# Kernel optimization log

Hardware: AMD Instinct MI355X
Metric: run time of the kernel (lower is better)

Reference implementation:

```python
import jax, jax.numpy as jnp
import numpy as np

# Static DAG: input -> L hidden layers of K nodes (dense between layers) -> output.
B, WIDTH, K, L = 262144, 64, 4, 4


def _linear_init(key, shape, fan_in):
    # matches nn.Linear default: U(-1/sqrt(fan_in), 1/sqrt(fan_in))
    bound = 1.0 / np.sqrt(fan_in)
    return jax.random.uniform(key, shape, jnp.float32, -bound, bound)


def setup_inputs() -> dict:
    key = jax.random.key(0)
    ks = jax.random.split(key, 9)
    x = jax.random.normal(ks[0], (B, WIDTH), jnp.float32)
    # input node -> first hidden layer (K edges)
    W_in = _linear_init(ks[1], (K, WIDTH, WIDTH), WIDTH)
    b_in = _linear_init(ks[2], (K, WIDTH), WIDTH)
    # between hidden layers: (L-1) transitions, K*K edges each; [pred, node, out, in]
    W_mid = _linear_init(ks[3], (L - 1, K, K, WIDTH, WIDTH), WIDTH)
    b_mid = _linear_init(ks[4], (L - 1, K, K, WIDTH), WIDTH)
    # last hidden layer -> output node (K edges)
    W_out = _linear_init(ks[5], (K, WIDTH, WIDTH), WIDTH)
    b_out = _linear_init(ks[6], (K, WIDTH), WIDTH)
    return {"x": x, "W_in": W_in, "b_in": b_in, "W_mid": W_mid,
            "b_mid": b_mid, "W_out": W_out, "b_out": b_out}


def _l2_normalize(t):
    # torch.linalg.norm(t) with no dim: Frobenius norm over the WHOLE tensor
    return t / jnp.linalg.norm(t)


def reference(x, W_in, b_in, W_mid, b_mid, W_out, b_out):
    # input node -> layer 1: each node k gets a single edge Linear, then normalize
    h = jnp.einsum('bw,kvw->kbv', x, W_in) + b_in[:, None, :]  # [K,B,W]
    h = jax.vmap(_l2_normalize)(h)
    # hidden -> hidden transitions: node v sums over its K predecessor edges
    for l in range(L - 1):  # small fixed structural loop over layers
        pre = jnp.einsum('pbw,pkvw->kbv', h, W_mid[l]) + b_mid[l].sum(axis=0)[:, None, :]
        h = jax.vmap(_l2_normalize)(pre)
    # last layer -> output node: sum K edge outputs, normalize
    out = jnp.einsum('pbw,pvw->bv', h, W_out) + b_out.sum(axis=0)
    return _l2_normalize(out)
```

## Files before the change

kernel.cpp:

```cpp
#include <hip/hip_runtime.h>


#define BF 262144.0f

#define OFF_G     0
#define OFF_S     4096
#define OFF_Q1    4160
#define OFF_Q2    4224
#define OFF_Q3    4288
#define OFF_Q4    5312
#define OFF_N2    21696
#define OFF_COUT  21760
#define OFF_SV1   21824
#define OFF_SV2   22080
#define OFF_SV3   23104
#define OFF_SV4   27200
#define OFF_MO    43584
#define OFF_B0    47680
#define OFF_B1    47936
#define OFF_B2    48192
#define OFF_U2    48512
#define OFF_U3    49536
#define OFF_U4    53632
#define OFF_V3    70016
#define OFF_V4A   71040
#define OFF_V4B   75136
#define OFF_UO    76160
#define OFF_VOA   92544
#define OFF_VOB   96640
#define OFF_VOC   97664
#define OFF_P2    98304
#define OFF_P3    163840
#define OFF_P4    425984
#define OFF_PO    1474560
#define OFF_X16   2523136
#define NZERO     17600

typedef __attribute__((ext_vector_type(8))) short bf16x8;
typedef __attribute__((ext_vector_type(4))) float f32x4;
typedef __attribute__((ext_vector_type(4))) unsigned short u16x4;

__device__ __forceinline__ unsigned short f2bf(float f) {
  unsigned u = __builtin_bit_cast(unsigned, f);
  u += 0x7FFF + ((u >> 16) & 1);
  return (unsigned short)(u >> 16);
}

__device__ __forceinline__ bf16x8 cvt8(f32x4 a, f32x4 b, float s) {
  bf16x8 t;
#pragma unroll
  for (int j = 0; j < 4; j++) {
    t[j]     = (short)f2bf(a[j] * s);
    t[j + 4] = (short)f2bf(b[j] * s);
  }
  return t;
}

__device__ __forceinline__ void ld64(float* dst, const float* __restrict__ src, int tid) {
#pragma unroll
  for (int m = 0; m < 4; m++) {
    const int li = m * 1024 + tid * 4;
    *(f32x4*)&dst[(li >> 6) * 68 + (li & 63)] = *(const f32x4*)(src + li);
  }
}
__device__ __forceinline__ void st64(float* __restrict__ dst, const float* src, int tid) {
#pragma unroll
  for (int m = 0; m < 4; m++) {
    const int li = m * 1024 + tid * 4;
    *(f32x4*)(dst + li) = *(const f32x4*)&src[(li >> 6) * 68 + (li & 63)];
  }
}
__device__ __forceinline__ void mm64(float* C, const float* A, const float* B, int tid) {
  const int v0 = (tid >> 4) * 4, w0 = (tid & 15) * 4;
  f32x4 a0 = {0.f,0.f,0.f,0.f}, a1 = a0, a2 = a0, a3 = a0;
#pragma unroll 8
  for (int u = 0; u < 64; u++) {
    const f32x4 b = *(const f32x4*)&B[u * 68 + w0];
    a0 += b * A[(v0 + 0) * 68 + u];
    a1 += b * A[(v0 + 1) * 68 + u];
    a2 += b * A[(v0 + 2) * 68 + u];
    a3 += b * A[(v0 + 3) * 68 + u];
  }
  *(f32x4*)&C[(v0 + 0) * 68 + w0] = a0;
  *(f32x4*)&C[(v0 + 1) * 68 + w0] = a1;
  *(f32x4*)&C[(v0 + 2) * 68 + w0] = a2;
  *(f32x4*)&C[(v0 + 3) * 68 + w0] = a3;
}
__device__ __forceinline__ void mv64(float* dst, const float* W, const float* vec,
                                     float (*red)[64], int tid) {
  const int v = tid & 63, q = tid >> 6;
  float p = 0.f;
#pragma unroll
  for (int u = q * 16; u < q * 16 + 16; u++) p += W[v * 68 + u] * vec[u];
  red[q][v] = p;
  __syncthreads();
  if (tid < 64) dst[tid] = red[0][tid] + red[1][tid] + red[2][tid] + red[3][tid];
  __syncthreads();
}

__global__ __launch_bounds__(256) void kGP(const float* __restrict__ x,
                                           float* __restrict__ Gpart,
                                           unsigned short* __restrict__ x16,
                                           const float* __restrict__ Win,
                                           const float* __restrict__ bin,
                                           const float* __restrict__ Wmid,
                                           const float* __restrict__ bmid,
                                           const float* __restrict__ Wout,
                                           float* __restrict__ ws) {
  __shared__ __align__(16) char shm[3 * 4352 * 4];
  __shared__ float vbuf[14][64];
  __shared__ float red4v[4][64];
  const int tid = threadIdx.x;

  if (blockIdx.x < 512) {
    typedef unsigned short xts_t[4][16][8];
    xts_t* xts = (xts_t*)shm;
    float (*sred)[4] = (float(*)[4])(shm + 4096);
    const int lane = tid & 63, mt = tid >> 6;
    const int col = lane & 15, q = lane >> 4;
    const int row0 = tid >> 4;
    const int cf0  = (tid & 15) * 4;

    f32x4 acc[4];
#pragma unroll
    for (int nt = 0; nt < 4; nt++) acc[nt] = (f32x4){0.f, 0.f, 0.f, 0.f};
    float s0 = 0.f, s1 = 0.f, s2 = 0.f, s3 = 0.f;

    const long brow = (long)blockIdx.x * 512;
    const float* bx = x + brow * 64;
    f32x4 r0 = *(const f32x4*)(bx + tid * 4);
    f32x4 r1 = *(const f32x4*)(bx + 1024 + tid * 4);

    for (int c = 0; c < 16; c++) {
      __syncthreads();
      s0 += r0[0] + r1[0]; s1 += r0[1] + r1[1];
      s2 += r0[2] + r1[2]; s3 += r0[3] + r1[3];
      u16x4 h0, h1;
#pragma unroll
      for (int j = 0; j < 4; j++) {
        const int cf = cf0 + j;
        const unsigned short b0 = f2bf(r0[j]);
        const unsigned short b1 = f2bf(r1[j]);
        h0[j] = b0; h1[j] = b1;
        xts[cf >> 4][row0 >> 3][cf & 15][row0 & 7]        = b0;
        xts[cf >> 4][2 + (row0 >> 3)][cf & 15][row0 & 7]  = b1;
      }
      *(u16x4*)(x16 + (brow + c * 32 + row0) * 64 + cf0)      = h0;
      *(u16x4*)(x16 + (brow + c * 32 + 16 + row0) * 64 + cf0) = h1;
      f32x4 r0n = r0, r1n = r1;
      if (c < 15) {
        r0n = *(const f32x4*)(bx + (c + 1) * 2048 + tid * 4);
        r1n = *(const f32x4*)(bx + (c + 1) * 2048 + 1024 + tid * 4);
      }
      __syncthreads();
      const bf16x8 af = *(const bf16x8*)xts[mt][q][col];
#pragma unroll
      for (int nt = 0; nt < 4; nt++) {
        const bf16x8 bfr = *(const bf16x8*)xts[nt][q][col];
        acc[nt] = __builtin_amdgcn_mfma_f32_16x16x32_bf16(af, bfr, acc[nt], 0, 0, 0);
      }
      r0 = r0n; r1 = r1n;
    }

    float* myp = Gpart + (long)blockIdx.x * 4160;
#pragma unroll
    for (int nt = 0; nt < 4; nt++)
#pragma unroll
      for (int r = 0; r < 4; r++)
        myp[(mt * 16 + q * 4 + r) * 64 + nt * 16 + col] = acc[nt][r];

    sred[tid][0] = s0; sred[tid][1] = s1; sred[tid][2] = s2; sred[tid][3] = s3;
    __syncthreads();
    if (tid < 64) {
      float t = 0.f;
#pragma unroll
      for (int k2 = 0; k2 < 16; k2++) t += sred[(tid >> 2) + 16 * k2][tid & 3];
      myp[4096 + tid] = t;
    }
  } else {
    float* mb0 = (float*)shm;
    float* mb1 = mb0 + 4352;
    float* mb2 = mb1 + 4352;
    float* binl = vbuf[0]; float* B0l = vbuf[1]; float* B1l = vbuf[2]; float* B2l = vbuf[3];
    float* u2 = vbuf[4];  float* u3 = vbuf[5];  float* v3 = vbuf[6];
    float* u4 = vbuf[7];  float* v4a = vbuf[8]; float* v4b = vbuf[9];
    float* uo = vbuf[10]; float* voa = vbuf[11]; float* vob = vbuf[12]; float* voc = vbuf[13];
    const int pid = blockIdx.x - 512;
    const int p1 = (pid >> 6) & 3, p2 = (pid >> 4) & 3, p3 = (pid >> 2) & 3, p4 = pid & 3;
    const float* bm0 = bmid;
    const float* bm1 = bmid + 1024;
    const float* bm2 = bmid + 2048;

    if (tid < 64) {
      binl[tid] = bin[p1 * 64 + tid];
      B0l[tid] = bm0[(0*4+p2)*64+tid] + bm0[(1*4+p2)*64+tid] + bm0[(2*4+p2)*64+tid] + bm0[(3*4+p2)*64+tid];
      B1l[tid] = bm1[(0*4+p3)*64+tid] + bm1[(1*4+p3)*64+tid] + bm1[(2*4+p3)*64+tid] + bm1[(3*4+p3)*64+tid];
      B2l[tid] = bm2[(0*4+p4)*64+tid] + bm2[(1*4+p4)*64+tid] + bm2[(2*4+p4)*64+tid] + bm2[(3*4+p4)*64+tid];
    }
    ld64(mb0, Win + p1 * 4096, tid);
    ld64(mb1, Wmid + (p1 * 4 + p2) * 4096, tid);
    __syncthreads();
    mv64(u2, mb1, binl, red4v, tid);
    mm64(mb2, mb1, mb0, tid);
    __syncthreads();
    if (p3 == 0 && p4 == 0) {
      st64(ws + OFF_P2 + (p1 * 4 + p2) * 4096, mb2, tid);
      if (tid < 64) ws[OFF_U2 + (p1 * 4 + p2) * 64 + tid] = u2[tid];
    }
    ld64(mb1, Wmid + 65536 + (p2 * 4 + p3) * 4096, tid);
    __syncthreads();
    mv64(u3, mb1, u2, red4v, tid);
    mv64(v3, mb1, B0l, red4v, tid);
    mm64(mb0, mb1, mb2, tid);
    __syncthreads();
    if (p4 == 0) {
      st64(ws + OFF_P3 + (p1 * 16 + p2 * 4 + p3) * 4096, mb0, tid);
      if (tid < 64) ws[OFF_U3 + (p1 * 16 + p2 * 4 + p3) * 64 + tid] = u3[tid];
      if (p1 == 0 && tid < 64) ws[OFF_V3 + (p2 * 4 + p3) * 64 + tid] = v3[tid];
    }
    ld64(mb1, Wmid + 131072 + (p3 * 4 + p4) * 4096, tid);
    __syncthreads();
    mv64(u4, mb1, u3, red4v, tid);
    mv64(v4a, mb1, v3, red4v, tid);
    mv64(v4b, mb1, B1l, red4v, tid);
    mm64(mb2, mb1, mb0, tid);
    __syncthreads();
    st64(ws + OFF_P4 + pid * 4096, mb2, tid);
    if (tid < 64) {
      ws[OFF_U4 + pid * 64 + tid] = u4[tid];
      if (p1 == 0) ws[OFF_V4A + ((p2 * 4 + p3) * 4 + p4) * 64 + tid] = v4a[tid];
      if (p1 == 0 && p2 == 0) ws[OFF_V4B + (p3 * 4 + p4) * 64 + tid] = v4b[tid];
    }
    ld64(mb1, Wout + p4 * 4096, tid);
    __syncthreads();
    mv64(uo, mb1, u4, red4v, tid);
    mv64(voa, mb1, v4a, red4v, tid);
    mv64(vob, mb1, v4b, red4v, tid);
    mv64(voc, mb1, B2l, red4v, tid);
    mm64(mb0, mb1, mb2, tid);
    __syncthreads();
    st64(ws + OFF_PO + pid * 4096, mb0, tid);
    if (tid < 64) {
      ws[OFF_UO + pid * 64 + tid] = uo[tid];
      if (p1 == 0) ws[OFF_VOA + ((p2 * 4 + p3) * 4 + p4) * 64 + tid] = voa[tid];
      if (p1 == 0 && p2 == 0) ws[OFF_VOB + (p3 * 4 + p4) * 64 + tid] = vob[tid];
      if (p1 == 0 && p2 == 0 && p3 == 0) ws[OFF_VOC + p4 * 64 + tid] = voc[tid];
    }
    if (pid == 0) {
      const int t = tid >> 6, v = tid & 63;
      ws[OFF_B0 + tid] = bm0[(0*4+t)*64+v] + bm0[(1*4+t)*64+v] + bm0[(2*4+t)*64+v] + bm0[(3*4+t)*64+v];
      ws[OFF_B1 + tid] = bm1[(0*4+t)*64+v] + bm1[(1*4+t)*64+v] + bm1[(2*4+t)*64+v] + bm1[(3*4+t)*64+v];
      ws[OFF_B2 + tid] = bm2[(0*4+t)*64+v] + bm2[(1*4+t)*64+v] + bm2[(2*4+t)*64+v] + bm2[(3*4+t)*64+v];
    }
  }
}

__global__ __launch_bounds__(256) void kGred(const float* __restrict__ Gpart,
                                             float* __restrict__ ws) {
  __shared__ float red[4][64];
  const int tid = threadIdx.x;
  for (int i = blockIdx.x * 256 + tid; i < NZERO; i += 65 * 256)
    ws[OFF_Q1 + i] = 0.f;
  const int e = blockIdx.x * 64 + (tid & 63);
  const int quarter = tid >> 6;
  float acc = 0.f;
#pragma unroll 4
  for (int j = 0; j < 128; j++)
    acc += Gpart[(long)(quarter * 128 + j) * 4160 + e];
  red[quarter][tid & 63] = acc;
  __syncthreads();
  if (tid < 64) {
    const float t = red[0][tid] + red[1][tid] + red[2][tid] + red[3][tid];
    const int ee = blockIdx.x * 64 + tid;
    if (ee < 4096) ws[OFF_G + ee] = t;
    else           ws[OFF_S + ee - 4096] = t;
  }
}

__global__ __launch_bounds__(256) void kTab(const float* __restrict__ Win,
                                            float* __restrict__ ws) {
  __shared__ __align__(16) float Gl[64 * 68];
  __shared__ __align__(16) float Al[64 * 68];
  __shared__ __align__(16) float Bl[64 * 68];
  __shared__ float red[256];
  __shared__ float sl[64];
  const int tid = threadIdx.x, b = blockIdx.x;
  const int it = tid >> 6, lane = tid & 63;

  ld64(Gl, ws + OFF_G, tid);
  if (tid < 64) sl[tid] = ws[OFF_S + tid];
  __syncthreads();

  if (b < 4) {
    ld64(Al, Win + b * 4096, tid);
    __syncthreads();
    const int vq = it, w = lane;
    float part = 0.f;
    for (int m = 0; m < 16; m++) {
      const int v = vq + m * 4;
      float bw = 0.f;
#pragma unroll 8
      for (int wp = 0; wp < 64; wp++) bw += Al[v * 68 + wp] * Gl[wp * 68 + w];
      part += bw * Al[v * 68 + w];
    }
    red[tid] = part;
    __syncthreads();
    for (int st = 128; st > 0; st >>= 1) {
      if (tid < st) red[tid] += red[tid + st];
      __syncthreads();
    }
    if (tid == 0) ws[OFF_Q1 + b] = red[0];
  } else if (b < 164) {
    int NP, nv, v0, node, qoff;
    const float* Pbase;
    if (b < 20)      { NP = 4;  node = (b - 4)  >> 2; v0 = ((b - 4)  & 3) * 16; nv = 16; Pbase = ws + OFF_P2; qoff = OFF_Q2 + node * 16; }
    else if (b < 36) { NP = 16; node = (b - 20) >> 2; v0 = ((b - 20) & 3) * 16; nv = 16; Pbase = ws + OFF_P3; qoff = OFF_Q3 + node * 256; }
    else             { NP = 64; node = (b - 36) >> 5; v0 = ((b - 36) & 31) * 2; nv = 2;  Pbase = ws + OFF_P4; qoff = OFF_Q4 + node * 4096; }

    float q1acc = 0.f;
    f32x4 qq0 = {0.f,0.f,0.f,0.f}, qq1 = qq0, qq2 = qq0, qq3 = qq0;

    for (int vi = 0; vi < nv; vi++) {
      const int v = v0 + vi;
      __syncthreads();
      for (int e = tid * 4; e < NP * 64; e += 1024) {
        const int j = e >> 6, c = e & 63;
        *(f32x4*)&Al[j * 68 + c] = *(const f32x4*)(Pbase + (long)(j * 4 + node) * 4096 + v * 64 + c);
      }
      __syncthreads();
      if (NP == 64) {
        const int j = tid >> 2, w0 = (tid & 3) * 16;
        f32x4 a0 = {0.f,0.f,0.f,0.f}, a1 = a0, a2 = a0, a3 = a0;
#pragma unroll 8
        for (int wp = 0; wp < 64; wp++) {
          const float a = Al[j * 68 + wp];
          a0 += a * *(const f32x4*)&Gl[wp * 68 + w0];
          a1 += a * *(const f32x4*)&Gl[wp * 68 + w0 + 4];
          a2 += a * *(const f32x4*)&Gl[wp * 68 + w0 + 8];
          a3 += a * *(const f32x4*)&Gl[wp * 68 + w0 + 12];
        }
        *(f32x4*)&Bl[j * 68 + w0]      = a0;
        *(f32x4*)&Bl[j * 68 + w0 + 4]  = a1;
        *(f32x4*)&Bl[j * 68 + w0 + 8]  = a2;
        *(f32x4*)&Bl[j * 68 + w0 + 12] = a3;
      } else if (NP == 16) {
        const int j = tid >> 4, w0 = (tid & 15) * 4;
        f32x4 a0 = {0.f,0.f,0.f,0.f};
#pragma unroll 8
        for (int wp = 0; wp < 64; wp++)
          a0 += Al[j * 68 + wp] * *(const f32x4*)&Gl[wp * 68 + w0];
        *(f32x4*)&Bl[j * 68 + w0] = a0;
      } else {
        const int j = tid >> 6, w = tid & 63;
        float a0 = 0.f;
#pragma unroll 8
        for (int wp = 0; wp < 64; wp++) a0 += Al[j * 68 + wp] * Gl[wp * 68 + w];
        Bl[j * 68 + w] = a0;
      }
      __syncthreads();
      if (NP == 64) {
        const int j0 = (tid >> 4) * 4, jp = tid & 15;
#pragma unroll 4
        for (int w4 = 0; w4 < 16; w4++) {
          const f32x4 b0 = *(const f32x4*)&Bl[(j0 + 0) * 68 + w4 * 4];
          const f32x4 b1 = *(const f32x4*)&Bl[(j0 + 1) * 68 + w4 * 4];
          const f32x4 b2 = *(const f32x4*)&Bl[(j0 + 2) * 68 + w4 * 4];
          const f32x4 b3 = *(const f32x4*)&Bl[(j0 + 3) * 68 + w4 * 4];
#pragma unroll
          for (int bb = 0; bb < 4; bb++) {
            const f32x4 av = *(const f32x4*)&Al[(jp + 16 * bb) * 68 + w4 * 4];
            qq0[bb] += b0[0]*av[0] + b0[1]*av[1] + b0[2]*av[2] + b0[3]*av[3];
            qq1[bb] += b1[0]*av[0] + b1[1]*av[1] + b1[2]*av[2] + b1[3]*av[3];
            qq2[bb] += b2[0]*av[0] + b2[1]*av[1] + b2[2]*av[2] + b2[3]*av[3];
            qq3[bb] += b3[0]*av[0] + b3[1]*av[1] + b3[2]*av[2] + b3[3]*av[3];
          }
        }
      } else if (NP == 16) {
        const int j = tid >> 4, jp = tid & 15;
#pragma unroll 4
        for (int w4 = 0; w4 < 16; w4++) {
          const f32x4 bv = *(const f32x4*)&Bl[j * 68 + w4 * 4];
          const f32x4 av = *(const f32x4*)&Al[jp * 68 + w4 * 4];
          q1acc += bv[0]*av[0] + bv[1]*av[1] + bv[2]*av[2] + bv[3]*av[3];
        }
      } else {
        if (tid < 16) {
          const int j = tid >> 2, jp = tid & 3;
#pragma unroll 8
          for (int w = 0; w < 64; w++) q1acc += Bl[j * 68 + w] * Al[jp * 68 + w];
        }
      }
    }
    if (NP == 64) {
      const int j0 = (tid >> 4) * 4, jp = tid & 15;
#pragma unroll
      for (int bb = 0; bb < 4; bb++) {
        atomicAdd(&ws[qoff + (j0 + 0) * 64 + jp + 16 * bb], qq0[bb]);
        atomicAdd(&ws[qoff + (j0 + 1) * 64 + jp + 16 * bb], qq1[bb]);
        atomicAdd(&ws[qoff + (j0 + 2) * 64 + jp + 16 * bb], qq2[bb]);
        atomicAdd(&ws[qoff + (j0 + 3) * 64 + jp + 16 * bb], qq3[bb]);
      }
    } else if (NP == 16) {
      atomicAdd(&ws[qoff + (tid >> 4) * 16 + (tid & 15)], q1acc);
    } else if (tid < 16) {
      atomicAdd(&ws[qoff + tid], q1acc);
    }
  } else {
    const int vb = b - 164;
    const int lo = vb * 85, hi = (vb == 3) ? 340 : lo + 85;
    for (int vec = lo + it; vec < hi; vec += 4) {
      const float* mat; int dst;
      if (vec < 4)       { mat = Win + vec * 4096;                dst = OFF_SV1 + vec * 64; }
      else if (vec < 20) { mat = ws + OFF_P2 + (vec - 4) * 4096;  dst = OFF_SV2 + (vec - 4) * 64; }
      else if (vec < 84) { mat = ws + OFF_P3 + (vec - 20) * 4096; dst = OFF_SV3 + (vec - 20) * 64; }
      else               { mat = ws + OFF_P4 + (vec - 84) * 4096; dst = OFF_SV4 + (vec - 84) * 64; }
      float acc = 0.f;
#pragma unroll
      for (int u4 = 0; u4 < 16; u4++) {
        const f32x4 mv = *(const f32x4*)(mat + lane * 64 + u4 * 4);
        acc += mv[0]*sl[u4*4] + mv[1]*sl[u4*4+1] + mv[2]*sl[u4*4+2] + mv[3]*sl[u4*4+3];
      }
      ws[dst + lane] = acc;
    }
  }
}

__global__ __launch_bounds__(256) void kLM(
    const float* __restrict__ bin, const float* __restrict__ bout,
    float* __restrict__ ws) {
  __shared__ float binl[256], c2l[256], c3l[256], c4l[256], col[64];
  __shared__ float sv1l[256], sv2l[1024];
  __shared__ float inv1[4], inv2[4], inv3[4], inv4[4];
  __shared__ float C2l[4], C3l[16], C4l[64], mco[256];
  __shared__ __align__(16) float Grow[64 * 68];
  __shared__ float sl[64];
  __shared__ float tfl[4][64];
  __shared__ float redb[256];
  const int tid = threadIdx.x, it = tid >> 6, lane = tid & 63;

  binl[tid] = bin[tid];
  sv1l[tid] = ws[OFF_SV1 + tid];
#pragma unroll
  for (int m = 0; m < 4; m++) sv2l[m * 256 + tid] = ws[OFF_SV2 + m * 256 + tid];
  if (tid < 64) sl[tid] = ws[OFF_S + tid];
  ld64(Grow, ws + OFF_G, tid);
  __syncthreads();

  {
    const float c = binl[it * 64 + lane];
    float part = c * (2.f * sv1l[it * 64 + lane] + BF * c);
#pragma unroll
    for (int off = 32; off; off >>= 1) part += __shfl_down(part, off, 64);
    if (lane == 0) inv1[it] = rsqrtf(ws[OFF_Q1 + it] + part);
  }
  __syncthreads();
  if (tid < 4) C2l[tid] = inv1[tid];
  __syncthreads();
  {
    float acc = ws[OFF_B0 + it * 64 + lane];
#pragma unroll
    for (int p1 = 0; p1 < 4; p1++)
      acc += inv1[p1] * ws[OFF_U2 + (p1 * 4 + it) * 64 + lane];
    c2l[it * 64 + lane] = acc;
  }
  __syncthreads();
  {
    float ts = 0.f;
#pragma unroll
    for (int p1 = 0; p1 < 4; p1++) ts += C2l[p1] * sv2l[(p1 * 4 + it) * 64 + lane];
    const float c = c2l[it * 64 + lane];
    float part = c * (2.f * ts + BF * c);
    if (lane < 16) part += C2l[lane >> 2] * C2l[lane & 3] * ws[OFF_Q2 + it * 16 + lane];
#pragma unroll
    for (int off = 32; off; off >>= 1) part += __shfl_down(part, off, 64);
    if (lane == 0) inv2[it] = rsqrtf(part);
  }
  __syncthreads();
  if (tid < 16) C3l[tid] = C2l[tid >> 2] * inv2[tid & 3];
  __syncthreads();
  {
    float acc = ws[OFF_B1 + it * 64 + lane];
#pragma unroll
    for (int p2 = 0; p2 < 4; p2++) {
      float tmp = ws[OFF_V3 + (p2 * 4 + it) * 64 + lane];
#pragma unroll
      for (int p1 = 0; p1 < 4; p1++)
        tmp += inv1[p1] * ws[OFF_U3 + ((p1 * 4 + p2) * 4 + it) * 64 + lane];
      acc += inv2[p2] * tmp;
    }
    c3l[it * 64 + lane] = acc;
  }
  __syncthreads();
  {
    float ts = 0.f;
#pragma unroll
    for (int j = 0; j < 16; j++) ts += C3l[j] * ws[OFF_SV3 + (j * 4 + it) * 64 + lane];
    const float c = c3l[it * 64 + lane];
    float part = c * (2.f * ts + BF * c);
#pragma unroll
    for (int k = 0; k < 4; k++) {
      const int idx = lane * 4 + k;
      part += C3l[idx >> 4] * C3l[idx & 15] * ws[OFF_Q3 + it * 256 + idx];
    }
#pragma unroll
    for (int off = 32; off; off >>= 1) part += __shfl_down(part, off, 64);
    if (lane == 0) inv3[it] = rsqrtf(part);
  }
  __syncthreads();
  if (tid < 64) C4l[tid] = C3l[tid >> 2] * inv3[tid & 3];
  __syncthreads();
  {
    float acc = ws[OFF_B2 + it * 64 + lane];
#pragma unroll
    for (int p3 = 0; p3 < 4; p3++) {
      float t3 = ws[OFF_V4B + (p3 * 4 + it) * 64 + lane];
#pragma unroll
      for (int p2 = 0; p2 < 4; p2++) {
        float t2 = ws[OFF_V4A + ((p2 * 4 + p3) * 4 + it) * 64 + lane];
#pragma unroll
        for (int p1 = 0; p1 < 4; p1++)
          t2 += inv1[p1] * ws[OFF_U4 + (((p1 * 4 + p2) * 4 + p3) * 4 + it) * 64 + lane];
        t3 += inv2[p2] * t2;
      }
      acc += inv3[p3] * t3;
    }
    c4l[it * 64 + lane] = acc;
  }
  __syncthreads();
  {
    float ts = 0.f;
    for (int j = 0; j < 64; j++) ts += C4l[j] * ws[OFF_SV4 + (j * 4 + it) * 64 + lane];
    const float c = c4l[it * 64 + lane];
    float part = c * (2.f * ts + BF * c);
    float colv = 0.f;
#pragma unroll 8
    for (int j = 0; j < 64; j++)
      colv += C4l[j] * ws[OFF_Q4 + it * 4096 + j * 64 + lane];
    part += C4l[lane] * colv;
#pragma unroll
    for (int off = 32; off; off >>= 1) part += __shfl_down(part, off, 64);
    if (lane == 0) inv4[it] = rsqrtf(part);
  }
  __syncthreads();
  mco[tid] = C4l[tid >> 2] * inv4[tid & 3];
  {
    float acc = ws[OFF_VOC + it * 64 + lane];
#pragma unroll
    for (int p3 = 0; p3 < 4; p3++) {
      float t3 = ws[OFF_VOB + (p3 * 4 + it) * 64 + lane];
#pragma unroll
      for (int p2 = 0; p2 < 4; p2++) {
        float t2 = ws[OFF_VOA + ((p2 * 4 + p3) * 4 + it) * 64 + lane];
#pragma unroll
        for (int p1 = 0; p1 < 4; p1++)
          t2 += inv1[p1] * ws[OFF_UO + (((p1 * 4 + p2) * 4 + p3) * 4 + it) * 64 + lane];
        t3 += inv2[p2] * t2;
      }
      acc += inv3[p3] * t3;
    }
    c2l[it * 64 + lane] = inv4[it] * acc + bout[it * 64 + lane];
  }
  __syncthreads();
  if (tid < 64) col[tid] = c2l[tid] + c2l[64 + tid] + c2l[128 + tid] + c2l[192 + tid];
  __syncthreads();
  if (blockIdx.x == 0 && tid < 64) ws[OFF_COUT + tid] = col[tid];

  const int v = blockIdx.x * 4 + it;
  {
    float acc = 0.f;
    const float* po = ws + OFF_PO + v * 64 + lane;
#pragma unroll 4
    for (int i = 0; i < 256; i++) acc += mco[i] * po[(long)i * 4096];
    tfl[it][lane] = acc;
    ws[OFF_MO + v * 64 + lane] = acc;
  }
  __syncthreads();
  {
    float bw = 0.f;
#pragma unroll 8
    for (int wp = 0; wp < 64; wp++) bw += tfl[it][wp] * Grow[wp * 68 + lane];
    float part = bw * tfl[it][lane] + 2.f * col[v] * tfl[it][lane] * sl[lane];
    redb[tid] = part;
    __syncthreads();
    for (int st = 128; st > 0; st >>= 1) {
      if (tid < st) redb[tid] += redb[tid + st];
      __syncthreads();
    }
    if (tid == 0) atomicAdd(&ws[OFF_N2], redb[0]);
    if (blockIdx.x == 0 && it == 0) {
      float p2_ = BF * col[lane] * col[lane];
#pragma unroll
      for (int off = 32; off; off >>= 1) p2_ += __shfl_down(p2_, off, 64);
      if (lane == 0) atomicAdd(&ws[OFF_N2], p2_);
    }
  }
}

__global__ __launch_bounds__(256) void kApply(const unsigned short* __restrict__ x16,
                                              const float* __restrict__ MoU,
                                              const float* __restrict__ coU,
                                              const float* __restrict__ n2p,
                                              float* __restrict__ out) {
  const int tid = threadIdx.x, lane = tid & 63, vt = tid >> 6;
  const int col = lane & 15, q = lane >> 4;
  const float inv = rsqrtf(n2p[0]);

  bf16x8 bfr[2];
  const float* mr = MoU + (vt * 16 + col) * 64 + q * 8;
  bfr[0] = cvt8(*(const f32x4*)mr, *(const f32x4*)(mr + 4), inv);
  bfr[1] = cvt8(*(const f32x4*)(mr + 32), *(const f32x4*)(mr + 36), inv);
  const float cf = inv * coU[vt * 16 + col];

  for (int t = 0; t < 16; t++) {
    const int b0 = (blockIdx.x * 16 + t) * 16;
    const unsigned short* xr = x16 + (long)(b0 + col) * 64 + q * 8;
    const bf16x8 a0 = *(const bf16x8*)xr;
    const bf16x8 a1 = *(const bf16x8*)(xr + 32);
    f32x4 acc = (f32x4){0.f, 0.f, 0.f, 0.f};
    acc = __builtin_amdgcn_mfma_f32_16x16x32_bf16(a0, bfr[0], acc, 0, 0, 0);
    acc = __builtin_amdgcn_mfma_f32_16x16x32_bf16(a1, bfr[1], acc, 0, 0, 0);
#pragma unroll
    for (int r = 0; r < 4; r++)
      out[(long)(b0 + q * 4 + r) * 64 + vt * 16 + col] = acc[r] + cf;
  }
}

extern "C" void kernel_launch(void* const* d_in, const int* in_sizes, int n_in,
                              void* d_out, int out_size, void* d_ws, size_t ws_size,
                              hipStream_t stream) {
  const float* x    = (const float*)d_in[0];
  const float* Win  = (const float*)d_in[1];
  const float* bin  = (const float*)d_in[2];
  const float* Wmid = (const float*)d_in[3];
  const float* bmid = (const float*)d_in[4];
  const float* Wout = (const float*)d_in[5];
  const float* bout = (const float*)d_in[6];
  float* out = (float*)d_out;
  float* ws  = (float*)d_ws;
  float* Gpart = out;
  unsigned short* x16 = (unsigned short*)(ws + OFF_X16);

  kGP  <<<768, 256, 0, stream>>>(x, Gpart, x16, Win, bin, Wmid, bmid, Wout, ws);
  kGred<<<65, 256, 0, stream>>>(Gpart, ws);
  kTab <<<168, 256, 0, stream>>>(Win, ws);
  kLM  <<<16, 256, 0, stream>>>(bin, bout, ws);
  kApply<<<1024, 256, 0, stream>>>(x16, ws + OFF_MO, ws + OFF_COUT, ws + OFF_N2, out);
}
```

Before: 242.6 us.

## Fuse kTab and kLM into one launch with atomic done-counter spin wait

```diff
diff --git a/kernel.cpp b/kernel.cpp
--- a/kernel.cpp
+++ b/kernel.cpp
@@ -10,6 +10,7 @@
 #define OFF_Q3    4288
 #define OFF_Q4    5312
 #define OFF_N2    21696
+#define OFF_DONE  21704
 #define OFF_COUT  21760
 #define OFF_SV1   21824
 #define OFF_SV2   22080
@@ -277,321 +278,344 @@
   }
 }
 
-__global__ __launch_bounds__(256) void kTab(const float* __restrict__ Win,
-                                            float* __restrict__ ws) {
-  __shared__ __align__(16) float Gl[64 * 68];
-  __shared__ __align__(16) float Al[64 * 68];
-  __shared__ __align__(16) float Bl[64 * 68];
-  __shared__ float red[256];
-  __shared__ float sl[64];
+__global__ __launch_bounds__(256) void kTabLM(const float* __restrict__ Win,
+                                              const float* __restrict__ bin,
+                                              const float* __restrict__ bout,
+                                              float* __restrict__ ws) {
+  __shared__ __align__(16) char sm[53504];
   const int tid = threadIdx.x, b = blockIdx.x;
   const int it = tid >> 6, lane = tid & 63;
 
-  ld64(Gl, ws + OFF_G, tid);
-  if (tid < 64) sl[tid] = ws[OFF_S + tid];
-  __syncthreads();
-
-  if (b < 4) {
-    ld64(Al, Win + b * 4096, tid);
-    __syncthreads();
-    const int vq = it, w = lane;
-    float part = 0.f;
-    for (int m = 0; m < 16; m++) {
-      const int v = vq + m * 4;
+  if (b < 168) {
+    float* Gl = (float*)sm;
+    float* Al = Gl + 4352;
+    float* Bl = Al + 4352;
+    float* red = (float*)(sm + 52224);
+    float* sl  = red + 256;
+
+    ld64(Gl, ws + OFF_G, tid);
+    if (tid < 64) sl[tid] = ws[OFF_S + tid];
+    __syncthreads();
+
+    if (b < 4) {
+      ld64(Al, Win + b * 4096, tid);
+      __syncthreads();
+      const int vq = it, w = lane;
+      float part = 0.f;
+      for (int m = 0; m < 16; m++) {
+        const int v = vq + m * 4;
+        float bw = 0.f;
+#pragma unroll 8
+        for (int wp = 0; wp < 64; wp++) bw += Al[v * 68 + wp] * Gl[wp * 68 + w];
+        part += bw * Al[v * 68 + w];
+      }
+      red[tid] = part;
+      __syncthreads();
+      for (int st = 128; st > 0; st >>= 1) {
+        if (tid < st) red[tid] += red[tid + st];
+        __syncthreads();
+      }
+      if (tid == 0) ws[OFF_Q1 + b] = red[0];
+    } else if (b < 164) {
+      int NP, nv, v0, node, qoff;
+      const float* Pbase;
+      if (b < 20)      { NP = 4;  node = (b - 4)  >> 2; v0 = ((b - 4)  & 3) * 16; nv = 16; Pbase = ws + OFF_P2; qoff = OFF_Q2 + node * 16; }
+      else if (b < 36) { NP = 16; node = (b - 20) >> 2; v0 = ((b - 20) & 3) * 16; nv = 16; Pbase = ws + OFF_P3; qoff = OFF_Q3 + node * 256; }
+      else             { NP = 64; node = (b - 36) >> 5; v0 = ((b - 36) & 31) * 2; nv = 2;  Pbase = ws + OFF_P4; qoff = OFF_Q4 + node * 4096; }
+
+      float q1acc = 0.f;
+      f32x4 qq0 = {0.f,0.f,0.f,0.f}, qq1 = qq0, qq2 = qq0, qq3 = qq0;
+
+      for (int vi = 0; vi < nv; vi++) {
+        const int v = v0 + vi;
+        __syncthreads();
+        for (int e = tid * 4; e < NP * 64; e += 1024) {
+          const int j = e >> 6, c = e & 63;
+          *(f32x4*)&Al[j * 68 + c] = *(const f32x4*)(Pbase + (long)(j * 4 + node) * 4096 + v * 64 + c);
+        }
+        __syncthreads();
+        if (NP == 64) {
+          const int j0 = (tid >> 4) * 4, w0 = (tid & 15) * 4;
+          f32x4 c0 = {0.f,0.f,0.f,0.f}, c1 = c0, c2 = c0, c3 = c0;
+#pragma unroll 4
+          for (int wp0 = 0; wp0 < 64; wp0 += 4) {
+            const f32x4 a0v = *(const f32x4*)&Al[(j0 + 0) * 68 + wp0];
+            const f32x4 a1v = *(const f32x4*)&Al[(j0 + 1) * 68 + wp0];
+            const f32x4 a2v = *(const f32x4*)&Al[(j0 + 2) * 68 + wp0];
+            const f32x4 a3v = *(const f32x4*)&Al[(j0 + 3) * 68 + wp0];
+#pragma unroll
+            for (int k = 0; k < 4; k++) {
+              const f32x4 gv = *(const f32x4*)&Gl[(wp0 + k) * 68 + w0];
+              c0 += a0v[k] * gv; c1 += a1v[k] * gv;
+              c2 += a2v[k] * gv; c3 += a3v[k] * gv;
+            }
+          }
+          *(f32x4*)&Bl[(j0 + 0) * 68 + w0] = c0;
+          *(f32x4*)&Bl[(j0 + 1) * 68 + w0] = c1;
+          *(f32x4*)&Bl[(j0 + 2) * 68 + w0] = c2;
+          *(f32x4*)&Bl[(j0 + 3) * 68 + w0] = c3;
+        } else if (NP == 16) {
+          const int j = tid >> 4, w0 = (tid & 15) * 4;
+          f32x4 a0 = {0.f,0.f,0.f,0.f};
+#pragma unroll 4
+          for (int wp0 = 0; wp0 < 64; wp0 += 4) {
+            const f32x4 av = *(const f32x4*)&Al[j * 68 + wp0];
+#pragma unroll
+            for (int k = 0; k < 4; k++)
+              a0 += av[k] * *(const f32x4*)&Gl[(wp0 + k) * 68 + w0];
+          }
+          *(f32x4*)&Bl[j * 68 + w0] = a0;
+        } else {
+          const int j = tid >> 6, w = tid & 63;
+          float a0 = 0.f;
+#pragma unroll 8
+          for (int wp = 0; wp < 64; wp++) a0 += Al[j * 68 + wp] * Gl[wp * 68 + w];
+          Bl[j * 68 + w] = a0;
+        }
+        __syncthreads();
+        if (NP == 64) {
+          const int j0 = (tid >> 4) * 4, jp = tid & 15;
+#pragma unroll 4
+          for (int w4 = 0; w4 < 16; w4++) {
+            const f32x4 b0 = *(const f32x4*)&Bl[(j0 + 0) * 68 + w4 * 4];
+            const f32x4 b1 = *(const f32x4*)&Bl[(j0 + 1) * 68 + w4 * 4];
+            const f32x4 b2 = *(const f32x4*)&Bl[(j0 + 2) * 68 + w4 * 4];
+            const f32x4 b3 = *(const f32x4*)&Bl[(j0 + 3) * 68 + w4 * 4];
+#pragma unroll
+            for (int bb = 0; bb < 4; bb++) {
+              const f32x4 av = *(const f32x4*)&Al[(jp + 16 * bb) * 68 + w4 * 4];
+              qq0[bb] += b0[0]*av[0] + b0[1]*av[1] + b0[2]*av[2] + b0[3]*av[3];
+              qq1[bb] += b1[0]*av[0] + b1[1]*av[1] + b1[2]*av[2] + b1[3]*av[3];
+              qq2[bb] += b2[0]*av[0] + b2[1]*av[1] + b2[2]*av[2] + b2[3]*av[3];
+              qq3[bb] += b3[0]*av[0] + b3[1]*av[1] + b3[2]*av[2] + b3[3]*av[3];
+            }
+          }
+        } else if (NP == 16) {
+          const int j = tid >> 4, jp = tid & 15;
+#pragma unroll 4
+          for (int w4 = 0; w4 < 16; w4++) {
+            const f32x4 bv = *(const f32x4*)&Bl[j * 68 + w4 * 4];
+            const f32x4 av = *(const f32x4*)&Al[jp * 68 + w4 * 4];
+            q1acc += bv[0]*av[0] + bv[1]*av[1] + bv[2]*av[2] + bv[3]*av[3];
+          }
+        } else {
+          if (tid < 16) {
+            const int j = tid >> 2, jp = tid & 3;
+#pragma unroll 8
+            for (int w = 0; w < 64; w++) q1acc += Bl[j * 68 + w] * Al[jp * 68 + w];
+          }
+        }
+      }
+      if (NP == 64) {
+        const int j0 = (tid >> 4) * 4, jp = tid & 15;
+#pragma unroll
+        for (int bb = 0; bb < 4; bb++) {
+          atomicAdd(&ws[qoff + (j0 + 0) * 64 + jp + 16 * bb], qq0[bb]);
+          atomicAdd(&ws[qoff + (j0 + 1) * 64 + jp + 16 * bb], qq1[bb]);
+          atomicAdd(&ws[qoff + (j0 + 2) * 64 + jp + 16 * bb], qq2[bb]);
+          atomicAdd(&ws[qoff + (j0 + 3) * 64 + jp + 16 * bb], qq3[bb]);
+        }
+      } else if (NP == 16) {
+        atomicAdd(&ws[qoff + (tid >> 4) * 16 + (tid & 15)], q1acc);
+      } else if (tid < 16) {
+        atomicAdd(&ws[qoff + tid], q1acc);
+      }
+    } else {
+      const int vb = b - 164;
+      const int lo = vb * 85, hi = (vb == 3) ? 340 : lo + 85;
+      for (int vec = lo + it; vec < hi; vec += 4) {
+        const float* mat; int dst;
+        if (vec < 4)       { mat = Win + vec * 4096;                dst = OFF_SV1 + vec * 64; }
+        else if (vec < 20) { mat = ws + OFF_P2 + (vec - 4) * 4096;  dst = OFF_SV2 + (vec - 4) * 64; }
+        else if (vec < 84) { mat = ws + OFF_P3 + (vec - 20) * 4096; dst = OFF_SV3 + (vec - 20) * 64; }
+        else               { mat = ws + OFF_P4 + (vec - 84) * 4096; dst = OFF_SV4 + (vec - 84) * 64; }
+        float acc = 0.f;
+#pragma unroll
+        for (int u4 = 0; u4 < 16; u4++) {
+          const f32x4 mv = *(const f32x4*)(mat + lane * 64 + u4 * 4);
+          acc += mv[0]*sl[u4*4] + mv[1]*sl[u4*4+1] + mv[2]*sl[u4*4+2] + mv[3]*sl[u4*4+3];
+        }
+        ws[dst + lane] = acc;
+      }
+    }
+    __threadfence();
+    __syncthreads();
+    if (tid == 0) atomicAdd((unsigned*)&ws[OFF_DONE], 1u);
+  } else {
+    float* Grow = (float*)sm;
+    float* fp   = (float*)(sm + 17408);
+    float* binl = fp;        float* c2l = fp + 256;  float* c3l = fp + 512;
+    float* c4l  = fp + 768;  float* sv1l = fp + 1024; float* mco = fp + 1280;
+    float* redb = fp + 1536; float* sv2l = fp + 1792;
+    float* tfl  = fp + 2816;
+    float* col  = fp + 3072;
+    float* sl   = fp + 3136;
+    float* inv1 = fp + 3200; float* inv2 = inv1 + 4;
+    float* inv3 = inv2 + 4;  float* inv4 = inv3 + 4;
+    float* C2l  = fp + 3216; float* C3l = fp + 3220; float* C4l = fp + 3236;
+    const int bid = b - 168;
+
+    binl[tid] = bin[tid];
+    if (tid < 64) sl[tid] = ws[OFF_S + tid];
+    ld64(Grow, ws + OFF_G, tid);
+    if (tid == 0) {
+      while (__hip_atomic_load((unsigned*)&ws[OFF_DONE], __ATOMIC_ACQUIRE,
+                               __HIP_MEMORY_SCOPE_AGENT) < 168u) {}
+    }
+    __syncthreads();
+    __threadfence();
+    sv1l[tid] = ws[OFF_SV1 + tid];
+#pragma unroll
+    for (int m = 0; m < 4; m++) sv2l[m * 256 + tid] = ws[OFF_SV2 + m * 256 + tid];
+    __syncthreads();
+
+    {
+      const float c = binl[it * 64 + lane];
+      float part = c * (2.f * sv1l[it * 64 + lane] + BF * c);
+#pragma unroll
+      for (int off = 32; off; off >>= 1) part += __shfl_down(part, off, 64);
+      if (lane == 0) inv1[it] = rsqrtf(ws[OFF_Q1 + it] + part);
+    }
+    __syncthreads();
+    if (tid < 4) C2l[tid] = inv1[tid];
+    __syncthreads();
+    {
+      float acc = ws[OFF_B0 + it * 64 + lane];
+#pragma unroll
+      for (int p1 = 0; p1 < 4; p1++)
+        acc += inv1[p1] * ws[OFF_U2 + (p1 * 4 + it) * 64 + lane];
+      c2l[it * 64 + lane] = acc;
+    }
+    __syncthreads();
+    {
+      float ts = 0.f;
+#pragma unroll
+      for (int p1 = 0; p1 < 4; p1++) ts += C2l[p1] * sv2l[(p1 * 4 + it) * 64 + lane];
+      const float c = c2l[it * 64 + lane];
+      float part = c * (2.f * ts + BF * c);
+      if (lane < 16) part += C2l[lane >> 2] * C2l[lane & 3] * ws[OFF_Q2 + it * 16 + lane];
+#pragma unroll
+      for (int off = 32; off; off >>= 1) part += __shfl_down(part, off, 64);
+      if (lane == 0) inv2[it] = rsqrtf(part);
+    }
+    __syncthreads();
+    if (tid < 16) C3l[tid] = C2l[tid >> 2] * inv2[tid & 3];
+    __syncthreads();
+    {
+      float acc = ws[OFF_B1 + it * 64 + lane];
+#pragma unroll
+      for (int p2 = 0; p2 < 4; p2++) {
+        float tmp = ws[OFF_V3 + (p2 * 4 + it) * 64 + lane];
+#pragma unroll
+        for (int p1 = 0; p1 < 4; p1++)
+          tmp += inv1[p1] * ws[OFF_U3 + ((p1 * 4 + p2) * 4 + it) * 64 + lane];
+        acc += inv2[p2] * tmp;
+      }
+      c3l[it * 64 + lane] = acc;
+    }
+    __syncthreads();
+    {
+      float ts = 0.f;
+#pragma unroll
+      for (int j = 0; j < 16; j++) ts += C3l[j] * ws[OFF_SV3 + (j * 4 + it) * 64 + lane];
+      const float c = c3l[it * 64 + lane];
+      float part = c * (2.f * ts + BF * c);
+#pragma unroll
+      for (int k = 0; k < 4; k++) {
+        const int idx = lane * 4 + k;
+        part += C3l[idx >> 4] * C3l[idx & 15] * ws[OFF_Q3 + it * 256 + idx];
+      }
+#pragma unroll
+      for (int off = 32; off; off >>= 1) part += __shfl_down(part, off, 64);
+      if (lane == 0) inv3[it] = rsqrtf(part);
+    }
+    __syncthreads();
+    if (tid < 64) C4l[tid] = C3l[tid >> 2] * inv3[tid & 3];
+    __syncthreads();
+    {
+      float acc = ws[OFF_B2 + it * 64 + lane];
+#pragma unroll
+      for (int p3 = 0; p3 < 4; p3++) {
+        float t3 = ws[OFF_V4B + (p3 * 4 + it) * 64 + lane];
+#pragma unroll
+        for (int p2 = 0; p2 < 4; p2++) {
+          float t2 = ws[OFF_V4A + ((p2 * 4 + p3) * 4 + it) * 64 + lane];
+#pragma unroll
+          for (int p1 = 0; p1 < 4; p1++)
+            t2 += inv1[p1] * ws[OFF_U4 + (((p1 * 4 + p2) * 4 + p3) * 4 + it) * 64 + lane];
+          t3 += inv2[p2] * t2;
+        }
+        acc += inv3[p3] * t3;
+      }
+      c4l[it * 64 + lane] = acc;
+    }
+    __syncthreads();
+    {
+      float ts = 0.f;
+      for (int j = 0; j < 64; j++) ts += C4l[j] * ws[OFF_SV4 + (j * 4 + it) * 64 + lane];
+      const float c = c4l[it * 64 + lane];
+      float part = c * (2.f * ts + BF * c);
+      float colv = 0.f;
+#pragma unroll 8
+      for (int j = 0; j < 64; j++)
+        colv += C4l[j] * ws[OFF_Q4 + it * 4096 + j * 64 + lane];
+      part += C4l[lane] * colv;
+#pragma unroll
+      for (int off = 32; off; off >>= 1) part += __shfl_down(part, off, 64);
+      if (lane == 0) inv4[it] = rsqrtf(part);
+    }
+    __syncthreads();
+    mco[tid] = C4l[tid >> 2] * inv4[tid & 3];
+    {
+      float acc = ws[OFF_VOC + it * 64 + lane];
+#pragma unroll
+      for (int p3 = 0; p3 < 4; p3++) {
+        float t3 = ws[OFF_VOB + (p3 * 4 + it) * 64 + lane];
+#pragma unroll
+        for (int p2 = 0; p2 < 4; p2++) {
+          float t2 = ws[OFF_VOA + ((p2 * 4 + p3) * 4 + it) * 64 + lane];
+#pragma unroll
+          for (int p1 = 0; p1 < 4; p1++)
+            t2 += inv1[p1] * ws[OFF_UO + (((p1 * 4 + p2) * 4 + p3) * 4 + it) * 64 + lane];
+          t3 += inv2[p2] * t2;
+        }
+        acc += inv3[p3] * t3;
+      }
+      c2l[it * 64 + lane] = inv4[it] * acc + bout[it * 64 + lane];
+    }
+    __syncthreads();
+    if (tid < 64) col[tid] = c2l[tid] + c2l[64 + tid] + c2l[128 + tid] + c2l[192 + tid];
+    __syncthreads();
+    if (bid == 0 && tid < 64) ws[OFF_COUT + tid] = col[tid];
+
+    const int v = bid * 4 + it;
+    {
+      float acc = 0.f;
+      const float* po = ws + OFF_PO + v * 64 + lane;
+#pragma unroll 4
+      for (int i = 0; i < 256; i++) acc += mco[i] * po[(long)i * 4096];
+      tfl[it * 64 + lane] = acc;
+      ws[OFF_MO + v * 64 + lane] = acc;
+    }
+    __syncthreads();
+    {
       float bw = 0.f;
 #pragma unroll 8
-      for (int wp = 0; wp < 64; wp++) bw += Al[v * 68 + wp] * Gl[wp * 68 + w];
-      part += bw * Al[v * 68 + w];
-    }
-    red[tid] = part;
-    __syncthreads();
-    for (int st = 128; st > 0; st >>= 1) {
-      if (tid < st) red[tid] += red[tid + st];
+      for (int wp = 0; wp < 64; wp++) bw += tfl[it * 64 + wp] * Grow[wp * 68 + lane];
+      float part = bw * tfl[it * 64 + lane] + 2.f * col[v] * tfl[it * 64 + lane] * sl[lane];
+      redb[tid] = part;
       __syncthreads();
-    }
-    if (tid == 0) ws[OFF_Q1 + b] = red[0];
-  } else if (b < 164) {
-    int NP, nv, v0, node, qoff;
-    const float* Pbase;
-    if (b < 20)      { NP = 4;  node = (b - 4)  >> 2; v0 = ((b - 4)  & 3) * 16; nv = 16; Pbase = ws + OFF_P2; qoff = OFF_Q2 + node * 16; }
-    else if (b < 36) { NP = 16; node = (b - 20) >> 2; v0 = ((b - 20) & 3) * 16; nv = 16; Pbase = ws + OFF_P3; qoff = OFF_Q3 + node * 256; }
-    else             { NP = 64; node = (b - 36) >> 5; v0 = ((b - 36) & 31) * 2; nv = 2;  Pbase = ws + OFF_P4; qoff = OFF_Q4 + node * 4096; }
-
-    float q1acc = 0.f;
-    f32x4 qq0 = {0.f,0.f,0.f,0.f}, qq1 = qq0, qq2 = qq0, qq3 = qq0;
-
-    for (int vi = 0; vi < nv; vi++) {
-      const int v = v0 + vi;
-      __syncthreads();
-      for (int e = tid * 4; e < NP * 64; e += 1024) {
-        const int j = e >> 6, c = e & 63;
-        *(f32x4*)&Al[j * 68 + c] = *(const f32x4*)(Pbase + (long)(j * 4 + node) * 4096 + v * 64 + c);
-      }
-      __syncthreads();
-      if (NP == 64) {
-        const int j = tid >> 2, w0 = (tid & 3) * 16;
-        f32x4 a0 = {0.f,0.f,0.f,0.f}, a1 = a0, a2 = a0, a3 = a0;
-#pragma unroll 8
-        for (int wp = 0; wp < 64; wp++) {
-          const float a = Al[j * 68 + wp];
-          a0 += a * *(const f32x4*)&Gl[wp * 68 + w0];
-          a1 += a * *(const f32x4*)&Gl[wp * 68 + w0 + 4];
-          a2 += a * *(const f32x4*)&Gl[wp * 68 + w0 + 8];
-          a3 += a * *(const f32x4*)&Gl[wp * 68 + w0 + 12];
-        }
-        *(f32x4*)&Bl[j * 68 + w0]      = a0;
-        *(f32x4*)&Bl[j * 68 + w0 + 4]  = a1;
-        *(f32x4*)&Bl[j * 68 + w0 + 8]  = a2;
-        *(f32x4*)&Bl[j * 68 + w0 + 12] = a3;
-      } else if (NP == 16) {
-        const int j = tid >> 4, w0 = (tid & 15) * 4;
-        f32x4 a0 = {0.f,0.f,0.f,0.f};
-#pragma unroll 8
-        for (int wp = 0; wp < 64; wp++)
-          a0 += Al[j * 68 + wp] * *(const f32x4*)&Gl[wp * 68 + w0];
-        *(f32x4*)&Bl[j * 68 + w0] = a0;
-      } else {
-        const int j = tid >> 6, w = tid & 63;
-        float a0 = 0.f;
-#pragma unroll 8
-        for (int wp = 0; wp < 64; wp++) a0 += Al[j * 68 + wp] * Gl[wp * 68 + w];
-        Bl[j * 68 + w] = a0;
-      }
-      __syncthreads();
-      if (NP == 64) {
-        const int j0 = (tid >> 4) * 4, jp = tid & 15;
-#pragma unroll 4
-        for (int w4 = 0; w4 < 16; w4++) {
-          const f32x4 b0 = *(const f32x4*)&Bl[(j0 + 0) * 68 + w4 * 4];
-          const f32x4 b1 = *(const f32x4*)&Bl[(j0 + 1) * 68 + w4 * 4];
-          const f32x4 b2 = *(const f32x4*)&Bl[(j0 + 2) * 68 + w4 * 4];
-          const f32x4 b3 = *(const f32x4*)&Bl[(j0 + 3) * 68 + w4 * 4];
-#pragma unroll
-          for (int bb = 0; bb < 4; bb++) {
-            const f32x4 av = *(const f32x4*)&Al[(jp + 16 * bb) * 68 + w4 * 4];
-            qq0[bb] += b0[0]*av[0] + b0[1]*av[1] + b0[2]*av[2] + b0[3]*av[3];
-            qq1[bb] += b1[0]*av[0] + b1[1]*av[1] + b1[2]*av[2] + b1[3]*av[3];
-            qq2[bb] += b2[0]*av[0] + b2[1]*av[1] + b2[2]*av[2] + b2[3]*av[3];
-            qq3[bb] += b3[0]*av[0] + b3[1]*av[1] + b3[2]*av[2] + b3[3]*av[3];
-          }
-        }
-      } else if (NP == 16) {
-        const int j = tid >> 4, jp = tid & 15;
-#pragma unroll 4
-        for (int w4 = 0; w4 < 16; w4++) {
-          const f32x4 bv = *(const f32x4*)&Bl[j * 68 + w4 * 4];
-          const f32x4 av = *(const f32x4*)&Al[jp * 68 + w4 * 4];
-          q1acc += bv[0]*av[0] + bv[1]*av[1] + bv[2]*av[2] + bv[3]*av[3];
-        }
-      } else {
-        if (tid < 16) {
-          const int j = tid >> 2, jp = tid & 3;
-#pragma unroll 8
-          for (int w = 0; w < 64; w++) q1acc += Bl[j * 68 + w] * Al[jp * 68 + w];
-        }
-      }
-    }
-    if (NP == 64) {
-      const int j0 = (tid >> 4) * 4, jp = tid & 15;
-#pragma unroll
-      for (int bb = 0; bb < 4; bb++) {
-        atomicAdd(&ws[qoff + (j0 + 0) * 64 + jp + 16 * bb], qq0[bb]);
-        atomicAdd(&ws[qoff + (j0 + 1) * 64 + jp + 16 * bb], qq1[bb]);
-        atomicAdd(&ws[qoff + (j0 + 2) * 64 + jp + 16 * bb], qq2[bb]);
-        atomicAdd(&ws[qoff + (j0 + 3) * 64 + jp + 16 * bb], qq3[bb]);
-      }
-    } else if (NP == 16) {
-      atomicAdd(&ws[qoff + (tid >> 4) * 16 + (tid & 15)], q1acc);
-    } else if (tid < 16) {
-      atomicAdd(&ws[qoff + tid], q1acc);
-    }
-  } else {
-    const int vb = b - 164;
-    const int lo = vb * 85, hi = (vb == 3) ? 340 : lo + 85;
-    for (int vec = lo + it; vec < hi; vec += 4) {
-      const float* mat; int dst;
-      if (vec < 4)       { mat = Win + vec * 4096;                dst = OFF_SV1 + vec * 64; }
-      else if (vec < 20) { mat = ws + OFF_P2 + (vec - 4) * 4096;  dst = OFF_SV2 + (vec - 4) * 64; }
-      else if (vec < 84) { mat = ws + OFF_P3 + (vec - 20) * 4096; dst = OFF_SV3 + (vec - 20) * 64; }
-      else               { mat = ws + OFF_P4 + (vec - 84) * 4096; dst = OFF_SV4 + (vec - 84) * 64; }
-      float acc = 0.f;
-#pragma unroll
-      for (int u4 = 0; u4 < 16; u4++) {
-        const f32x4 mv = *(const f32x4*)(mat + lane * 64 + u4 * 4);
-        acc += mv[0]*sl[u4*4] + mv[1]*sl[u4*4+1] + mv[2]*sl[u4*4+2] + mv[3]*sl[u4*4+3];
-      }
-      ws[dst + lane] = acc;
-    }
-  }
-}
-
-__global__ __launch_bounds__(256) void kLM(
-    const float* __restrict__ bin, const float* __restrict__ bout,
-    float* __restrict__ ws) {
-  __shared__ float binl[256], c2l[256], c3l[256], c4l[256], col[64];
-  __shared__ float sv1l[256], sv2l[1024];
-  __shared__ float inv1[4], inv2[4], inv3[4], inv4[4];
-  __shared__ float C2l[4], C3l[16], C4l[64], mco[256];
-  __shared__ __align__(16) float Grow[64 * 68];
-  __shared__ float sl[64];
-  __shared__ float tfl[4][64];
-  __shared__ float redb[256];
-  const int tid = threadIdx.x, it = tid >> 6, lane = tid & 63;
-
-  binl[tid] = bin[tid];
-  sv1l[tid] = ws[OFF_SV1 + tid];
-#pragma unroll
-  for (int m = 0; m < 4; m++) sv2l[m * 256 + tid] = ws[OFF_SV2 + m * 256 + tid];
-  if (tid < 64) sl[tid] = ws[OFF_S + tid];
-  ld64(Grow, ws + OFF_G, tid);
-  __syncthreads();
-
-  {
-    const float c = binl[it * 64 + lane];
-    float part = c * (2.f * sv1l[it * 64 + lane] + BF * c);
-#pragma unroll
-    for (int off = 32; off; off >>= 1) part += __shfl_down(part, off, 64);
-    if (lane == 0) inv1[it] = rsqrtf(ws[OFF_Q1 + it] + part);
-  }
-  __syncthreads();
-  if (tid < 4) C2l[tid] = inv1[tid];
-  __syncthreads();
-  {
-    float acc = ws[OFF_B0 + it * 64 + lane];
-#pragma unroll
-    for (int p1 = 0; p1 < 4; p1++)
-      acc += inv1[p1] * ws[OFF_U2 + (p1 * 4 + it) * 64 + lane];
-    c2l[it * 64 + lane] = acc;
-  }
-  __syncthreads();
-  {
-    float ts = 0.f;
-#pragma unroll
-    for (int p1 = 0; p1 < 4; p1++) ts += C2l[p1] * sv2l[(p1 * 4 + it) * 64 + lane];
-    const float c = c2l[it * 64 + lane];
-    float part = c * (2.f * ts + BF * c);
-    if (lane < 16) part += C2l[lane >> 2] * C2l[lane & 3] * ws[OFF_Q2 + it * 16 + lane];
-#pragma unroll
-    for (int off = 32; off; off >>= 1) part += __shfl_down(part, off, 64);
-    if (lane == 0) inv2[it] = rsqrtf(part);
-  }
-  __syncthreads();
-  if (tid < 16) C3l[tid] = C2l[tid >> 2] * inv2[tid & 3];
-  __syncthreads();
-  {
-    float acc = ws[OFF_B1 + it * 64 + lane];
-#pragma unroll
-    for (int p2 = 0; p2 < 4; p2++) {
-      float tmp = ws[OFF_V3 + (p2 * 4 + it) * 64 + lane];
-#pragma unroll
-      for (int p1 = 0; p1 < 4; p1++)
-        tmp += inv1[p1] * ws[OFF_U3 + ((p1 * 4 + p2) * 4 + it) * 64 + lane];
-      acc += inv2[p2] * tmp;
-    }
-    c3l[it * 64 + lane] = acc;
-  }
-  __syncthreads();
-  {
-    float ts = 0.f;
-#pragma unroll
-    for (int j = 0; j < 16; j++) ts += C3l[j] * ws[OFF_SV3 + (j * 4 + it) * 64 + lane];
-    const float c = c3l[it * 64 + lane];
-    float part = c * (2.f * ts + BF * c);
-#pragma unroll
-    for (int k = 0; k < 4; k++) {
-      const int idx = lane * 4 + k;
-      part += C3l[idx >> 4] * C3l[idx & 15] * ws[OFF_Q3 + it * 256 + idx];
-    }
-#pragma unroll
-    for (int off = 32; off; off >>= 1) part += __shfl_down(part, off, 64);
-    if (lane == 0) inv3[it] = rsqrtf(part);
-  }
-  __syncthreads();
-  if (tid < 64) C4l[tid] = C3l[tid >> 2] * inv3[tid & 3];
-  __syncthreads();
-  {
-    float acc = ws[OFF_B2 + it * 64 + lane];
-#pragma unroll
-    for (int p3 = 0; p3 < 4; p3++) {
-      float t3 = ws[OFF_V4B + (p3 * 4 + it) * 64 + lane];
-#pragma unroll
-      for (int p2 = 0; p2 < 4; p2++) {
-        float t2 = ws[OFF_V4A + ((p2 * 4 + p3) * 4 + it) * 64 + lane];
-#pragma unroll
-        for (int p1 = 0; p1 < 4; p1++)
-          t2 += inv1[p1] * ws[OFF_U4 + (((p1 * 4 + p2) * 4 + p3) * 4 + it) * 64 + lane];
-        t3 += inv2[p2] * t2;
-      }
-      acc += inv3[p3] * t3;
-    }
-    c4l[it * 64 + lane] = acc;
-  }
-  __syncthreads();
-  {
-    float ts = 0.f;
-    for (int j = 0; j < 64; j++) ts += C4l[j] * ws[OFF_SV4 + (j * 4 + it) * 64 + lane];
-    const float c = c4l[it * 64 + lane];
-    float part = c * (2.f * ts + BF * c);
-    float colv = 0.f;
-#pragma unroll 8
-    for (int j = 0; j < 64; j++)
-      colv += C4l[j] * ws[OFF_Q4 + it * 4096 + j * 64 + lane];
-    part += C4l[lane] * colv;
-#pragma unroll
-    for (int off = 32; off; off >>= 1) part += __shfl_down(part, off, 64);
-    if (lane == 0) inv4[it] = rsqrtf(part);
-  }
-  __syncthreads();
-  mco[tid] = C4l[tid >> 2] * inv4[tid & 3];
-  {
-    float acc = ws[OFF_VOC + it * 64 + lane];
-#pragma unroll
-    for (int p3 = 0; p3 < 4; p3++) {
-      float t3 = ws[OFF_VOB + (p3 * 4 + it) * 64 + lane];
-#pragma unroll
-      for (int p2 = 0; p2 < 4; p2++) {
-        float t2 = ws[OFF_VOA + ((p2 * 4 + p3) * 4 + it) * 64 + lane];
-#pragma unroll
-        for (int p1 = 0; p1 < 4; p1++)
-          t2 += inv1[p1] * ws[OFF_UO + (((p1 * 4 + p2) * 4 + p3) * 4 + it) * 64 + lane];
-        t3 += inv2[p2] * t2;
-      }
-      acc += inv3[p3] * t3;
-    }
-    c2l[it * 64 + lane] = inv4[it] * acc + bout[it * 64 + lane];
-  }
-  __syncthreads();
-  if (tid < 64) col[tid] = c2l[tid] + c2l[64 + tid] + c2l[128 + tid] + c2l[192 + tid];
-  __syncthreads();
-  if (blockIdx.x == 0 && tid < 64) ws[OFF_COUT + tid] = col[tid];
-
-  const int v = blockIdx.x * 4 + it;
-  {
-    float acc = 0.f;
-    const float* po = ws + OFF_PO + v * 64 + lane;
-#pragma unroll 4
-    for (int i = 0; i < 256; i++) acc += mco[i] * po[(long)i * 4096];
-    tfl[it][lane] = acc;
-    ws[OFF_MO + v * 64 + lane] = acc;
-  }
-  __syncthreads();
-  {
-    float bw = 0.f;
-#pragma unroll 8
-    for (int wp = 0; wp < 64; wp++) bw += tfl[it][wp] * Grow[wp * 68 + lane];
-    float part = bw * tfl[it][lane] + 2.f * col[v] * tfl[it][lane] * sl[lane];
-    redb[tid] = part;
-    __syncthreads();
-    for (int st = 128; st > 0; st >>= 1) {
-      if (tid < st) redb[tid] += redb[tid + st];
-      __syncthreads();
-    }
-    if (tid == 0) atomicAdd(&ws[OFF_N2], redb[0]);
-    if (blockIdx.x == 0 && it == 0) {
-      float p2_ = BF * col[lane] * col[lane];
-#pragma unroll
-      for (int off = 32; off; off >>= 1) p2_ += __shfl_down(p2_, off, 64);
-      if (lane == 0) atomicAdd(&ws[OFF_N2], p2_);
+      for (int st = 128; st > 0; st >>= 1) {
+        if (tid < st) redb[tid] += redb[tid + st];
+        __syncthreads();
+      }
+      if (tid == 0) atomicAdd(&ws[OFF_N2], redb[0]);
+      if (bid == 0 && it == 0) {
+        float p2_ = BF * col[lane] * col[lane];
+#pragma unroll
+        for (int off = 32; off; off >>= 1) p2_ += __shfl_down(p2_, off, 64);
+        if (lane == 0) atomicAdd(&ws[OFF_N2], p2_);
+      }
     }
   }
 }
@@ -640,9 +664,8 @@
   float* Gpart = out;
   unsigned short* x16 = (unsigned short*)(ws + OFF_X16);
 
-  kGP  <<<768, 256, 0, stream>>>(x, Gpart, x16, Win, bin, Wmid, bmid, Wout, ws);
-  kGred<<<65, 256, 0, stream>>>(Gpart, ws);
-  kTab <<<168, 256, 0, stream>>>(Win, ws);
-  kLM  <<<16, 256, 0, stream>>>(bin, bout, ws);
+  kGP   <<<768, 256, 0, stream>>>(x, Gpart, x16, Win, bin, Wmid, bmid, Wout, ws);
+  kGred <<<65, 256, 0, stream>>>(Gpart, ws);
+  kTabLM<<<184, 256, 0, stream>>>(Win, bin, bout, ws);
   kApply<<<1024, 256, 0, stream>>>(x16, ws + OFF_MO, ws + OFF_COUT, ws + OFF_N2, out);
 }
```

Result: slower. 254.4 us (+4.9%).
